# Kernel tuning notes

Hardware: AMD Instinct MI355X
Metric: run time of the kernel (lower is better)

## Reference

```python
import jax, jax.numpy as jnp
import numpy as np

MAX_RADIUS = 3.0
N_BASIS = 3
H = 100
C_IN = 23
N_ATOMS = 286
B = 32
Y0 = 1.0 / (2.0 * np.sqrt(np.pi))  # l=0 spherical harmonic


def cosine_basis(r):
    # e3nn CosineBasisModel basis: triangle-clamped then cosine bump
    radii = jnp.linspace(0.0, MAX_RADIUS, N_BASIS)
    step = radii[1] - radii[0]
    z = (r[..., None] - radii) / step                      # [..., N_BASIS]
    tri = 1.0 - jax.nn.relu(2.0 - jax.nn.relu(z + 1.0))    # clamp to [-1, 1]
    return jnp.cos(0.5 * jnp.pi * tri)


def setup_inputs() -> dict:
    key = jax.random.key(0)
    ks = jax.random.split(key, 10)
    def lin(k, fan_in, fan_out):
        return jax.random.normal(k, (fan_in, fan_out), jnp.float32) / np.sqrt(fan_in)
    return {
        "x": jax.random.normal(ks[0], (B, 1), jnp.float32),
        "features": jax.random.normal(ks[1], (B, N_ATOMS, C_IN), jnp.float32),
        "geometry": jax.random.normal(ks[2], (B, N_ATOMS, 3), jnp.float32),
        # radial MLP (CosineBasisModel, L=1 hidden layer of width h=100)
        "rW1": lin(ks[3], N_BASIS, H), "rb1": jnp.zeros((H,), jnp.float32),
        "rW2": lin(ks[4], H, C_IN),    "rb2": jnp.zeros((C_IN,), jnp.float32),
        # MLP head
        "fc1W": lin(ks[5], N_ATOMS, 30), "fc1b": jnp.zeros((30,), jnp.float32),
        "fc2W": lin(ks[6], 30, 10),      "fc2b": jnp.zeros((10,), jnp.float32),
        "fc3W": lin(ks[7], 10, 1),       "fc3b": jnp.zeros((1,), jnp.float32),
    }


def reference(x, features, geometry, rW1, rb1, rW2, rb2,
              fc1W, fc1b, fc2W, fc2b, fc3W, fc3b):
    Bz, N, _ = features.shape
    # pairwise distances r_ab = |geom_b - geom_a|, [B, N, N]
    diff = geometry[:, None, :, :] - geometry[:, :, None, :]
    r = jnp.sqrt(jnp.sum(diff * diff, axis=-1) + 1e-12)
    # radial kernel: cosine basis -> MLP -> 23 scalar-path weights per pair
    basis = cosine_basis(r)                                  # [B, N, N, 3]
    h = jax.nn.relu(basis @ rW1 + rb1)                       # [B, N, N, 100]
    R = (h @ rW2 + rb2) * Y0                                 # [B, N, N, 23]
    # scalar (l=0 -> l=0) point convolution, normalized by 1/sqrt(N)
    feats_new = jnp.einsum('zabj,zbj->za', R, features) * (1.0 / np.sqrt(N))
    # MLP head (fc1 consumes the [B, 286] conv output directly)
    out = jax.nn.relu(feats_new @ fc1W + fc1b)
    out = jax.nn.relu(out @ fc2W + fc2b)
    return out @ fc3W + fc3b                                 # [B, 1]
```

## Files before the change

### kernel.cpp

```cpp
#include <hip/hip_runtime.h>

#define NA      286
#define CIN     23
#define NKH     100
#define NKP     50
#define KPH     25
#define BATCH   32
#define NB_PAD  320
#define TB      64
#define ATILE   12
#define APW     3
#define NTILE_A 24
#define NTILE_B 5

#define Y0F      0.28209479177387814f
#define RSQRT_N  0.05913123960994873f

typedef _Float16 h2v __attribute__((ext_vector_type(2)));
union F4H { float4 f; h2v h[4]; };

__device__ __forceinline__ h2v h2_splat(float x) {
    _Float16 v = (_Float16)x;
    h2v r; r.x = v; r.y = v; return r;
}
__device__ __forceinline__ h2v h2_pack(float a, float b) {
    h2v r; r.x = (_Float16)a; r.y = (_Float16)b; return r;
}
__device__ __forceinline__ h2v h2_fma(h2v a, h2v b, h2v c) {
#if __has_builtin(__builtin_elementwise_fma)
    return __builtin_elementwise_fma(a, b, c);
#else
    return a * b + c;
#endif
}
__device__ __forceinline__ h2v h2_max0(h2v a) {
    h2v z; z.x = (_Float16)0.f; z.y = (_Float16)0.f;
#if __has_builtin(__builtin_elementwise_max)
    return __builtin_elementwise_max(a, z);
#else
    h2v r; r.x = a.x > z.x ? a.x : z.x; r.y = a.y > z.y ? a.y : z.y; return r;
#endif
}
__device__ __forceinline__ float fdot2f(h2v a, h2v b, float c) {
#if __has_builtin(__builtin_amdgcn_fdot2)
    return __builtin_amdgcn_fdot2(a, b, c, false);
#else
    return c + (float)a.x * (float)b.x + (float)a.y * (float)b.y;
#endif
}

__device__ __forceinline__ float cos_half_pi(float x) {
    float t = 1.5707963267948966f * x;
    float w = t * t;
    return 1.f + w * (-0.5f + w * (4.16666667e-2f + w * (-1.38888889e-3f
               + w * 2.48015873e-5f)));
}

__global__ void __launch_bounds__(256) prep_kernel(
    const float* __restrict__ feat,
    const float* __restrict__ rW2,
    const float* __restrict__ rW1,
    const float* __restrict__ rb1,
    h2v* __restrict__ cbuf2,
    float4* __restrict__ wpk)
{
    __shared__ float rlds[2 * KPH * CIN];
    const int tid = threadIdx.x;
    const int bT  = blockIdx.x;
    const int z   = blockIdx.y;
    const int kh  = blockIdx.z;

    if (bT == 0 && z == 0 && kh == 0 && tid < NKP) {
        int k0 = 2 * tid, k1 = k0 + 1;
        F4H u;
        u.h[0] = h2_pack(rW1[k0],           rW1[k1]);
        u.h[1] = h2_pack(rW1[NKH + k0],     rW1[NKH + k1]);
        u.h[2] = h2_pack(rW1[2 * NKH + k0], rW1[2 * NKH + k1]);
        u.h[3] = h2_pack(rb1[k0],           rb1[k1]);
        wpk[tid] = u.f;
    }

    const float* rsrc = rW2 + (size_t)kh * (NKH / 2) * CIN;
    for (int i = tid; i < 2 * KPH * CIN; i += 256) rlds[i] = rsrc[i];

    const int lane = tid & 63, wave = tid >> 6;
    const int b = bT * TB + lane;
    float f[CIN];
    if (b < NA) {
        const float* fp = feat + ((size_t)z * NA + b) * CIN;
#pragma unroll
        for (int j = 0; j < CIN; ++j) f[j] = fp[j];
    } else {
#pragma unroll
        for (int j = 0; j < CIN; ++j) f[j] = 0.f;
    }
    __syncthreads();

    for (int kp = wave; kp < KPH; kp += 4) {
        const float* w0 = &rlds[(2 * kp) * CIN];
        const float* w1 = &rlds[(2 * kp + 1) * CIN];
        float s0 = 0.f, s1 = 0.f;
#pragma unroll
        for (int j = 0; j < CIN; ++j) {
            s0 = fmaf(f[j], w0[j], s0);
            s1 = fmaf(f[j], w1[j], s1);
        }
        cbuf2[((size_t)z * NKP + kh * KPH + kp) * NB_PAD + bT * TB + lane] =
            h2_pack(s0 * Y0F, s1 * Y0F);
    }
}

__global__ void __launch_bounds__(256) pair_kernel(
    const float* __restrict__ geom,
    const h2v* __restrict__ cbuf2,
    const float4* __restrict__ wpk,
    float* __restrict__ feats_part)
{
    __shared__ h2v    c_lds[KPH * TB];
    __shared__ float4 wl[KPH];
    __shared__ float  ga[ATILE * 3];

    const int tid   = threadIdx.x;
    const int z     = blockIdx.y;
    const int kh    = blockIdx.z;
    const int aBase = blockIdx.x * ATILE;

    if (tid < KPH) wl[tid] = wpk[kh * KPH + tid];
    if (tid >= 64 && tid < 64 + ATILE * 3) {
        int t  = tid - 64;
        int aa = aBase + t / 3;
        int d  = t - 3 * (t / 3);
        ga[t] = (aa < NA) ? geom[((size_t)z * NA + aa) * 3 + d] : 0.f;
    }

    const int wave = tid >> 6;
    const int lane = tid & 63;

    float acc[APW] = {0.f, 0.f, 0.f};
    const h2v* csrc = cbuf2 + ((size_t)z * NKP + kh * KPH) * NB_PAD;

    for (int t = 0; t < NTILE_B; ++t) {
        const int b0 = t * TB;
        for (int i = tid; i < KPH * 16; i += 256) {
            int row = i >> 4, c4 = i & 15;
            uint4 v = *(const uint4*)(csrc + (size_t)row * NB_PAD + b0 + c4 * 4);
            *(uint4*)(&c_lds[row * TB + c4 * 4]) = v;
        }
        const int b = b0 + lane;
        float gbx = 0.f, gby = 0.f, gbz = 0.f;
        if (b < NA) {
            const float* g = geom + ((size_t)z * NA + b) * 3;
            gbx = g[0]; gby = g[1]; gbz = g[2];
        }
        __syncthreads();

        h2v u0[APW], u1[APW], u2[APW];
#pragma unroll
        for (int i = 0; i < APW; ++i) {
            const float* gp = &ga[(wave * APW + i) * 3];
            float dx = gbx - gp[0], dy = gby - gp[1], dz = gbz - gp[2];
            float r  = sqrtf(fmaf(dx, dx, fmaf(dy, dy, fmaf(dz, dz, 1e-12f))));
            float zz = r * (1.f / 1.5f);
            u0[i] = h2_splat(cos_half_pi(fminf(zz, 1.f)));
            u1[i] = h2_splat(cos_half_pi(fminf(fmaxf(zz - 1.f, -1.f), 1.f)));
            u2[i] = h2_splat(cos_half_pi(fminf(fmaxf(zz - 2.f, -1.f), 1.f)));
        }

#pragma unroll 5
        for (int kp = 0; kp < KPH; ++kp) {
            F4H u; u.f = wl[kp];
            h2v cb = c_lds[(kp << 6) | lane];
#pragma unroll
            for (int i = 0; i < APW; ++i) {
                h2v s = h2_fma(u0[i], u.h[0],
                        h2_fma(u1[i], u.h[1],
                        h2_fma(u2[i], u.h[2], u.h[3])));
                acc[i] = fdot2f(h2_max0(s), cb, acc[i]);
            }
        }
        __syncthreads();
    }

#pragma unroll
    for (int i = 0; i < APW; ++i) {
        float v = acc[i];
        for (int off = 32; off; off >>= 1) v += __shfl_xor(v, off);
        if (lane == 0) {
            int a = aBase + wave * APW + i;
            if (a < NA) feats_part[((size_t)kh * BATCH + z) * 288 + a] = v * RSQRT_N;
        }
    }
}

__global__ void __launch_bounds__(256) head_kernel(
    const float* __restrict__ featsP,
    const float* __restrict__ featIn,
    const float* __restrict__ rb2,
    const float* __restrict__ fc1W, const float* __restrict__ fc1b,
    const float* __restrict__ fc2W, const float* __restrict__ fc2b,
    const float* __restrict__ fc3W, const float* __restrict__ fc3b,
    float* __restrict__ out)
{
    __shared__ float fsum[NA];
    __shared__ float ps[8][CIN];
    __shared__ float po[8][30], pw[8][30];
    __shared__ float czs;
    __shared__ float h1[30], hh2[10];

    const int z = blockIdx.x, tid = threadIdx.x;

    for (int a = tid; a < NA; a += 256)
        fsum[a] = featsP[z * 288 + a] + featsP[(BATCH + z) * 288 + a];

    if (tid < 8 * CIN) {
        int j = tid % CIN, ch = tid / CIN;
        int b0 = ch * 36, b1 = (b0 + 36 < NA) ? b0 + 36 : NA;
        float s = 0.f;
        for (int b = b0; b < b1; ++b) s += featIn[((size_t)z * NA + b) * CIN + j];
        ps[ch][j] = s;
    }
    __syncthreads();
    if (tid < CIN) {
        float s = 0.f;
#pragma unroll
        for (int ch = 0; ch < 8; ++ch) s += ps[ch][tid];
        ps[0][tid] = s * rb2[tid];
    }
    __syncthreads();
    if (tid == 0) {
        float s = 0.f;
#pragma unroll
        for (int j = 0; j < CIN; ++j) s += ps[0][j];
        czs = s * (Y0F * RSQRT_N);
    }

    if (tid < 240) {
        int j = tid % 30, ch = tid / 30;
        int a0 = ch * 36, a1 = (a0 + 36 < NA) ? a0 + 36 : NA;
        float o = 0.f, ws = 0.f;
        for (int a = a0; a < a1; ++a) {
            float w = fc1W[a * 30 + j];
            o  = fmaf(fsum[a], w, o);
            ws += w;
        }
        po[ch][j] = o; pw[ch][j] = ws;
    }
    __syncthreads();
    if (tid < 30) {
        float o = 0.f, ws = 0.f;
#pragma unroll
        for (int ch = 0; ch < 8; ++ch) { o += po[ch][tid]; ws += pw[ch][tid]; }
        h1[tid] = fmaxf(o + czs * ws + fc1b[tid], 0.f);
    }
    __syncthreads();
    if (tid < 10) {
        float v = fc2b[tid];
#pragma unroll
        for (int t = 0; t < 30; ++t) v = fmaf(h1[t], fc2W[t * 10 + tid], v);
        hh2[tid] = fmaxf(v, 0.f);
    }
    __syncthreads();
    if (tid == 0) {
        float v = fc3b[0];
#pragma unroll
        for (int t = 0; t < 10; ++t) v = fmaf(hh2[t], fc3W[t], v);
        out[z] = v;
    }
}

extern "C" void kernel_launch(void* const* d_in, const int* in_sizes, int n_in,
                              void* d_out, int out_size, void* d_ws, size_t ws_size,
                              hipStream_t stream) {
    const float* features = (const float*)d_in[1];
    const float* geometry = (const float*)d_in[2];
    const float* rW1  = (const float*)d_in[3];
    const float* rb1  = (const float*)d_in[4];
    const float* rW2  = (const float*)d_in[5];
    const float* rb2  = (const float*)d_in[6];
    const float* fc1W = (const float*)d_in[7];
    const float* fc1b = (const float*)d_in[8];
    const float* fc2W = (const float*)d_in[9];
    const float* fc2b = (const float*)d_in[10];
    const float* fc3W = (const float*)d_in[11];
    const float* fc3b = (const float*)d_in[12];

    char* ws = (char*)d_ws;
    float4* wpk    = (float4*)ws;
    h2v*    cbuf2  = (h2v*)(ws + 1024);
    float*  featsP = (float*)(ws + 1024 + (size_t)BATCH * NKP * NB_PAD * 4);

    float* out = (float*)d_out;

    prep_kernel<<<dim3(NTILE_B, BATCH, 2), 256, 0, stream>>>(
        features, rW2, rW1, rb1, cbuf2, wpk);
    pair_kernel<<<dim3(NTILE_A, BATCH, 2), 256, 0, stream>>>(
        geometry, cbuf2, wpk, featsP);
    head_kernel<<<BATCH, 256, 0, stream>>>(
        featsP, features, rb2, fc1W, fc1b, fc2W, fc2b, fc3W, fc3b, out);
}
```

Measured before the change: 144.4 us.

## Stage features in LDS for prep and read pair coefficients directly from global

The prep kernel now loads a 64-atom feature tile and a smaller slice of rW2 cooperatively into LDS, and splits the k dimension over five blocks instead of two, so more blocks run and each does less work. The pair kernel drops its LDS staging of the coefficient tile and the radial weights along with both per-tile barriers. It reads the packed half2 coefficients and float4 weights straight from global/L2 inside the inner loop. This removes synchronization and LDS copies, but relies on cache hits for the repeated global loads in the hot loop.

```diff
diff --git a/kernel.cpp b/kernel.cpp
--- a/kernel.cpp
+++ b/kernel.cpp
@@ -12,6 +12,8 @@
 #define APW     3
 #define NTILE_A 24
 #define NTILE_B 5
+#define KQ_N    5
+#define KQ_SZ   10
 
 #define Y0F      0.28209479177387814f
 #define RSQRT_N  0.05913123960994873f
@@ -64,13 +66,14 @@
     h2v* __restrict__ cbuf2,
     float4* __restrict__ wpk)
 {
-    __shared__ float rlds[2 * KPH * CIN];
+    __shared__ float flds[TB * CIN];
+    __shared__ float wlds[2 * KQ_SZ * CIN];
     const int tid = threadIdx.x;
     const int bT  = blockIdx.x;
     const int z   = blockIdx.y;
-    const int kh  = blockIdx.z;
-
-    if (bT == 0 && z == 0 && kh == 0 && tid < NKP) {
+    const int kQ  = blockIdx.z;
+
+    if (bT == 0 && z == 0 && kQ == 0 && tid < NKP) {
         int k0 = 2 * tid, k1 = k0 + 1;
         F4H u;
         u.h[0] = h2_pack(rW1[k0],           rW1[k1]);
@@ -80,33 +83,30 @@
         wpk[tid] = u.f;
     }
 
-    const float* rsrc = rW2 + (size_t)kh * (NKH / 2) * CIN;
-    for (int i = tid; i < 2 * KPH * CIN; i += 256) rlds[i] = rsrc[i];
-
-    const int lane = tid & 63, wave = tid >> 6;
-    const int b = bT * TB + lane;
-    float f[CIN];
-    if (b < NA) {
-        const float* fp = feat + ((size_t)z * NA + b) * CIN;
-#pragma unroll
-        for (int j = 0; j < CIN; ++j) f[j] = fp[j];
-    } else {
-#pragma unroll
-        for (int j = 0; j < CIN; ++j) f[j] = 0.f;
-    }
-    __syncthreads();
-
-    for (int kp = wave; kp < KPH; kp += 4) {
-        const float* w0 = &rlds[(2 * kp) * CIN];
-        const float* w1 = &rlds[(2 * kp + 1) * CIN];
+    const int b0 = bT * TB;
+    const int nf = ((NA - b0 < TB) ? (NA - b0) : TB) * CIN;
+    const float* fsrc = feat + ((size_t)z * NA + b0) * CIN;
+    for (int i = tid; i < TB * CIN; i += 256)
+        flds[i] = (i < nf) ? fsrc[i] : 0.f;
+    const float* wsrc = rW2 + (size_t)kQ * KQ_SZ * 2 * CIN;
+    for (int i = tid; i < 2 * KQ_SZ * CIN; i += 256)
+        wlds[i] = wsrc[i];
+    __syncthreads();
+
+    for (int i = tid; i < TB * KQ_SZ; i += 256) {
+        int b   = i & 63;
+        int kpl = i >> 6;
+        const float* w0 = &wlds[(2 * kpl) * CIN];
+        const float* w1 = &wlds[(2 * kpl + 1) * CIN];
+        const float* fb = &flds[b * CIN];
         float s0 = 0.f, s1 = 0.f;
 #pragma unroll
         for (int j = 0; j < CIN; ++j) {
-            s0 = fmaf(f[j], w0[j], s0);
-            s1 = fmaf(f[j], w1[j], s1);
-        }
-        cbuf2[((size_t)z * NKP + kh * KPH + kp) * NB_PAD + bT * TB + lane] =
-            h2_pack(s0 * Y0F, s1 * Y0F);
+            s0 = fmaf(fb[j], w0[j], s0);
+            s1 = fmaf(fb[j], w1[j], s1);
+        }
+        int kp = kQ * KQ_SZ + kpl;
+        cbuf2[((size_t)z * NKP + kp) * NB_PAD + b0 + b] = h2_pack(s0 * Y0F, s1 * Y0F);
     }
 }
 
@@ -116,43 +116,34 @@
     const float4* __restrict__ wpk,
     float* __restrict__ feats_part)
 {
-    __shared__ h2v    c_lds[KPH * TB];
-    __shared__ float4 wl[KPH];
-    __shared__ float  ga[ATILE * 3];
+    __shared__ float ga[ATILE * 3];
 
     const int tid   = threadIdx.x;
     const int z     = blockIdx.y;
     const int kh    = blockIdx.z;
     const int aBase = blockIdx.x * ATILE;
 
-    if (tid < KPH) wl[tid] = wpk[kh * KPH + tid];
-    if (tid >= 64 && tid < 64 + ATILE * 3) {
-        int t  = tid - 64;
-        int aa = aBase + t / 3;
-        int d  = t - 3 * (t / 3);
-        ga[t] = (aa < NA) ? geom[((size_t)z * NA + aa) * 3 + d] : 0.f;
-    }
+    if (tid < ATILE * 3) {
+        int aa = aBase + tid / 3;
+        int d  = tid - 3 * (tid / 3);
+        ga[tid] = (aa < NA) ? geom[((size_t)z * NA + aa) * 3 + d] : 0.f;
+    }
+    __syncthreads();
 
     const int wave = tid >> 6;
     const int lane = tid & 63;
 
     float acc[APW] = {0.f, 0.f, 0.f};
-    const h2v* csrc = cbuf2 + ((size_t)z * NKP + kh * KPH) * NB_PAD;
+    const h2v*    csrc = cbuf2 + ((size_t)z * NKP + kh * KPH) * NB_PAD;
+    const float4* wsrc = wpk + kh * KPH;
 
     for (int t = 0; t < NTILE_B; ++t) {
-        const int b0 = t * TB;
-        for (int i = tid; i < KPH * 16; i += 256) {
-            int row = i >> 4, c4 = i & 15;
-            uint4 v = *(const uint4*)(csrc + (size_t)row * NB_PAD + b0 + c4 * 4);
-            *(uint4*)(&c_lds[row * TB + c4 * 4]) = v;
-        }
-        const int b = b0 + lane;
+        const int b = t * TB + lane;
         float gbx = 0.f, gby = 0.f, gbz = 0.f;
         if (b < NA) {
             const float* g = geom + ((size_t)z * NA + b) * 3;
             gbx = g[0]; gby = g[1]; gbz = g[2];
         }
-        __syncthreads();
 
         h2v u0[APW], u1[APW], u2[APW];
 #pragma unroll
@@ -166,10 +157,11 @@
             u2[i] = h2_splat(cos_half_pi(fminf(fmaxf(zz - 2.f, -1.f), 1.f)));
         }
 
+        const h2v* cp = csrc + t * TB + lane;
 #pragma unroll 5
         for (int kp = 0; kp < KPH; ++kp) {
-            F4H u; u.f = wl[kp];
-            h2v cb = c_lds[(kp << 6) | lane];
+            F4H u; u.f = wsrc[kp];
+            h2v cb = cp[(size_t)kp * NB_PAD];
 #pragma unroll
             for (int i = 0; i < APW; ++i) {
                 h2v s = h2_fma(u0[i], u.h[0],
@@ -178,7 +170,6 @@
                 acc[i] = fdot2f(h2_max0(s), cb, acc[i]);
             }
         }
-        __syncthreads();
     }
 
 #pragma unroll
@@ -291,7 +282,7 @@
 
     float* out = (float*)d_out;
 
-    prep_kernel<<<dim3(NTILE_B, BATCH, 2), 256, 0, stream>>>(
+    prep_kernel<<<dim3(NTILE_B, BATCH, KQ_N), 256, 0, stream>>>(
         features, rW2, rW1, rb1, cbuf2, wpk);
     pair_kernel<<<dim3(NTILE_A, BATCH, 2), 256, 0, stream>>>(
         geometry, cbuf2, wpk, featsP);
```

Measured after the change: 143.4 us. No clear change (-0.7%).
